# Kernel optimization log

Measured on AMD Instinct MI355X. Metric: run time of the kernel, lower is better.

Reference implementation:

```python
import jax, jax.numpy as jnp
import numpy as np

N_NODES = 50000
N_EDGES = 625000
D_IN = 128
D_OUT = 128


def setup_inputs() -> dict:
    key = jax.random.key(0)
    k1, k2, k3 = jax.random.split(key, 3)
    x = jax.random.normal(k1, (N_NODES, D_IN), dtype=jnp.float32)
    edge_index = jax.random.randint(k2, (2, N_EDGES), 0, N_NODES, dtype=jnp.int64)
    # torch Linear weight: [d_out, d_in], Kaiming-uniform-ish scale
    weight = jax.random.normal(k3, (D_OUT, D_IN), dtype=jnp.float32) * (1.0 / np.sqrt(D_IN))
    bias = jnp.zeros((D_OUT,), dtype=jnp.float32)
    return {"x": x, "edge_index": edge_index, "weight": weight, "bias": bias}


def reference(x, edge_index, weight, bias):
    N = x.shape[0]
    # gcn_norm: add self-loops with weight 1.0 (improved=False)
    loop = jnp.arange(N, dtype=edge_index.dtype)
    src = jnp.concatenate([edge_index[0], loop])  # [E+N] message sources (x_j)
    dst = jnp.concatenate([edge_index[1], loop])  # [E+N] aggregation targets
    ew = jnp.ones(src.shape[0], dtype=x.dtype)
    # degree computed on target index (col), symmetric normalization
    deg = jax.ops.segment_sum(ew, dst, num_segments=N)
    dinv = jnp.where(deg > 0, jax.lax.rsqrt(deg), 0.0).astype(x.dtype)
    norm = dinv[src] * ew * dinv[dst]  # [E+N]
    # message: norm_e * x[src]; aggregate: scatter-add at dst
    agg = jax.ops.segment_sum(norm[:, None] * x[src], dst, num_segments=N)  # [N, d_in]
    # Linear
    return agg @ weight.T + bias
```

## Files before the change

kernel.cpp:

```cpp
#include <hip/hip_runtime.h>
#include <hip/hip_bf16.h>

#define N_NODES 50000
#define N_EDGES 625000
#define D 128
#define CAP 64
#define NTILES ((N_NODES + 15) / 16)
#define NRANGE 8
#define RSPAN (N_NODES / NRANGE)
#define FILL_BLOCKS 1024
#define XW_BLOCKS 1024
#define PSTRIDE ((FILL_BLOCKS / NRANGE) * 256)

typedef __attribute__((ext_vector_type(8))) short bf16x8;
typedef __attribute__((ext_vector_type(4))) float f32x4;

__device__ __forceinline__ float b2f(short s) {
    unsigned u = ((unsigned)(unsigned short)s) << 16;
    return __uint_as_float(u);
}
__device__ __forceinline__ short f2b(float f) {
    union { __hip_bfloat16 h; short s; } cv;
    cv.h = __float2bfloat16(f);
    return cv.s;
}

__global__ void k_zero(int* __restrict__ deg) {
    int i = blockIdx.x * 256 + threadIdx.x;
    if (i < N_NODES) deg[i] = 0;
}

__global__ __launch_bounds__(256) void k_prep(const int* __restrict__ src,
                                              const int* __restrict__ dst,
                                              int* __restrict__ deg,
                                              unsigned short* __restrict__ colp,
                                              const float* __restrict__ x,
                                              const float* __restrict__ w,
                                              short* __restrict__ y) {
    int b = blockIdx.x;
    if (b < FILL_BLOCKS) {
        int g = b & 7;
        int bg = b >> 3;
        int lo = g * RSPAN, hi = lo + RSPAN;
        for (int e = bg * 256 + threadIdx.x; e < N_EDGES; e += PSTRIDE) {
            int d = dst[e];
            if (d >= lo && d < hi) {
                int p = atomicAdd(&deg[d], 1);
                if (p < CAP) colp[d * CAP + p] = (unsigned short)src[e];
            }
        }
    } else {
        int t = threadIdx.x;
        int wave = t >> 6, lane = t & 63;
        int c0 = wave * 32;
        int lr = lane & 15;
        int lk = (lane >> 4) * 8;

        bf16x8 wf0[4], wf1[4];
        {
            const float* wp0 = w + (size_t)(c0 + lr) * D + lk;
            const float* wp1 = wp0 + 16 * D;
            #pragma unroll
            for (int ks = 0; ks < 4; ++ks) {
                f32x4 wa0 = *(const f32x4*)(wp0 + ks * 32);
                f32x4 wb0 = *(const f32x4*)(wp0 + ks * 32 + 4);
                f32x4 wa1 = *(const f32x4*)(wp1 + ks * 32);
                f32x4 wb1 = *(const f32x4*)(wp1 + ks * 32 + 4);
                #pragma unroll
                for (int q = 0; q < 4; ++q) {
                    wf0[ks][q] = f2b(wa0[q]); wf0[ks][q + 4] = f2b(wb0[q]);
                    wf1[ks][q] = f2b(wa1[q]); wf1[ks][q + 4] = f2b(wb1[q]);
                }
            }
        }

        for (int tile = b - FILL_BLOCKS; tile < NTILES; tile += XW_BLOCKS) {
            int row0 = tile * 16;
            const float* ap = x + (size_t)(row0 + lr) * D + lk;
            f32x4 acc0 = {0.f, 0.f, 0.f, 0.f};
            f32x4 acc1 = {0.f, 0.f, 0.f, 0.f};
            #pragma unroll
            for (int ks = 0; ks < 4; ++ks) {
                f32x4 xa = *(const f32x4*)(ap + ks * 32);
                f32x4 xb = *(const f32x4*)(ap + ks * 32 + 4);
                bf16x8 a;
                #pragma unroll
                for (int q = 0; q < 4; ++q) { a[q] = f2b(xa[q]); a[q + 4] = f2b(xb[q]); }
                acc0 = __builtin_amdgcn_mfma_f32_16x16x32_bf16(a, wf0[ks], acc0, 0, 0, 0);
                acc1 = __builtin_amdgcn_mfma_f32_16x16x32_bf16(a, wf1[ks], acc1, 0, 0, 0);
            }
            int orow = row0 + (lane >> 4) * 4;
            int oc0 = c0 + lr, oc1 = c0 + 16 + lr;
            #pragma unroll
            for (int i = 0; i < 4; ++i) {
                y[(size_t)(orow + i) * D + oc0] = f2b(acc0[i]);
                y[(size_t)(orow + i) * D + oc1] = f2b(acc1[i]);
            }
        }
    }
}

__global__ __launch_bounds__(256) void k_gather(const short* __restrict__ y,
                                                const int* __restrict__ deg,
                                                const unsigned short* __restrict__ colp,
                                                const float* __restrict__ bias,
                                                float* __restrict__ out) {
    int tid = blockIdx.x * 256 + threadIdx.x;
    int n = tid >> 4;
    int sub = threadIdx.x & 15;
    int lane = threadIdx.x & 63;
    int gb = lane & 48;
    if (n >= N_NODES) return;
    int dn_raw = deg[n];
    float dd = rsqrtf((float)(dn_raw + 1));
    int dn = dn_raw < CAP ? dn_raw : CAP;
    bf16x8 self = *(const bf16x8*)(y + (size_t)n * D + sub * 8);
    float acc0[8], acc1[8];
    #pragma unroll
    for (int q = 0; q < 8; ++q) { acc0[q] = dd * b2f(self[q]); acc1[q] = 0.f; }
    const unsigned short* cp = colp + (size_t)n * CAP;

    for (int bj = 0; bj < dn; bj += 16) {
        int rem = dn - bj;
        int m = rem < 16 ? rem : 16;
        int cidx = 0;
        float cds = 0.f;
        if (sub < m) {
            cidx = cp[bj + sub];
            cds = rsqrtf((float)(deg[cidx] + 1));
        }
        int j = 0;
        for (; j + 4 <= m; j += 4) {
            int s0 = __shfl(cidx, gb + j + 0);
            int s1 = __shfl(cidx, gb + j + 1);
            int s2 = __shfl(cidx, gb + j + 2);
            int s3 = __shfl(cidx, gb + j + 3);
            float d0 = __shfl(cds, gb + j + 0);
            float d1 = __shfl(cds, gb + j + 1);
            float d2 = __shfl(cds, gb + j + 2);
            float d3 = __shfl(cds, gb + j + 3);
            bf16x8 v0 = *(const bf16x8*)(y + (size_t)s0 * D + sub * 8);
            bf16x8 v1 = *(const bf16x8*)(y + (size_t)s1 * D + sub * 8);
            bf16x8 v2 = *(const bf16x8*)(y + (size_t)s2 * D + sub * 8);
            bf16x8 v3 = *(const bf16x8*)(y + (size_t)s3 * D + sub * 8);
            #pragma unroll
            for (int q = 0; q < 8; ++q) {
                acc0[q] += d0 * b2f(v0[q]) + d2 * b2f(v2[q]);
                acc1[q] += d1 * b2f(v1[q]) + d3 * b2f(v3[q]);
            }
        }
        for (; j < m; ++j) {
            int s0 = __shfl(cidx, gb + j);
            float d0 = __shfl(cds, gb + j);
            bf16x8 v0 = *(const bf16x8*)(y + (size_t)s0 * D + sub * 8);
            #pragma unroll
            for (int q = 0; q < 8; ++q) acc0[q] += d0 * b2f(v0[q]);
        }
    }

    const float4* bch = (const float4*)(bias + sub * 8);
    float4 bb0 = bch[0], bb1 = bch[1];
    float4 o0, o1;
    o0.x = dd * (acc0[0] + acc1[0]) + bb0.x; o0.y = dd * (acc0[1] + acc1[1]) + bb0.y;
    o0.z = dd * (acc0[2] + acc1[2]) + bb0.z; o0.w = dd * (acc0[3] + acc1[3]) + bb0.w;
    o1.x = dd * (acc0[4] + acc1[4]) + bb1.x; o1.y = dd * (acc0[5] + acc1[5]) + bb1.y;
    o1.z = dd * (acc0[6] + acc1[6]) + bb1.z; o1.w = dd * (acc0[7] + acc1[7]) + bb1.w;
    float4* op = (float4*)(out + (size_t)n * D + sub * 8);
    op[0] = o0; op[1] = o1;
}

extern "C" void kernel_launch(void* const* d_in, const int* in_sizes, int n_in,
                              void* d_out, int out_size, void* d_ws, size_t ws_size,
                              hipStream_t stream) {
    const float* x    = (const float*)d_in[0];
    const int*   ei   = (const int*)d_in[1];
    const float* w    = (const float*)d_in[2];
    const float* bias = (const float*)d_in[3];
    float* out = (float*)d_out;

    const int* src = ei;
    const int* dst = ei + N_EDGES;

    char* p = (char*)d_ws;
    short* y  = (short*)p;             p += (size_t)N_NODES * D * 2;
    int* deg  = (int*)p;               p += (size_t)N_NODES * 4;
    unsigned short* colp = (unsigned short*)p;
    p += (size_t)N_NODES * CAP * 2;

    k_zero<<<(N_NODES + 255) / 256, 256, 0, stream>>>(deg);
    k_prep<<<FILL_BLOCKS + XW_BLOCKS, 256, 0, stream>>>(src, dst, deg, colp, x, w, y);
    k_gather<<<((N_NODES * 16) + 255) / 256, 256, 0, stream>>>(y, deg, colp, bias, out);
}
```

Measured before the change: 77.17 us.

## Assign edge-fill destination ranges by XCC with dynamic chunk work-stealing

The CSR fill phase used a static assignment where block b handled destination range b&7. Each fill block now reads its hardware XCC id and starts with the matching destination range, so the atomics on deg and the colp writes for a range stay mostly in one XCC's L2. Blocks take 2048-edge chunks from a per-range atomic cursor and move on to the other ranges when theirs is done, which balances load. The cost is extra global atomics and two barriers per chunk, and every block may end up scanning edges for several ranges.

```diff
diff --git a/kernel.cpp b/kernel.cpp
--- a/kernel.cpp
+++ b/kernel.cpp
@@ -10,7 +10,8 @@
 #define RSPAN (N_NODES / NRANGE)
 #define FILL_BLOCKS 1024
 #define XW_BLOCKS 1024
-#define PSTRIDE ((FILL_BLOCKS / NRANGE) * 256)
+#define CHUNK 2048
+#define NCHUNK ((N_EDGES + CHUNK - 1) / CHUNK)
 
 typedef __attribute__((ext_vector_type(8))) short bf16x8;
 typedef __attribute__((ext_vector_type(4))) float f32x4;
@@ -25,28 +26,47 @@
     return cv.s;
 }
 
-__global__ void k_zero(int* __restrict__ deg) {
+__global__ void k_zero(int* __restrict__ deg, int* __restrict__ cursor) {
     int i = blockIdx.x * 256 + threadIdx.x;
     if (i < N_NODES) deg[i] = 0;
+    if (i < NRANGE) cursor[i] = 0;
 }
 
 __global__ __launch_bounds__(256) void k_prep(const int* __restrict__ src,
                                               const int* __restrict__ dst,
                                               int* __restrict__ deg,
                                               unsigned short* __restrict__ colp,
+                                              int* __restrict__ cursor,
                                               const float* __restrict__ x,
                                               const float* __restrict__ w,
                                               short* __restrict__ y) {
     int b = blockIdx.x;
     if (b < FILL_BLOCKS) {
-        int g = b & 7;
-        int bg = b >> 3;
-        int lo = g * RSPAN, hi = lo + RSPAN;
-        for (int e = bg * 256 + threadIdx.x; e < N_EDGES; e += PSTRIDE) {
-            int d = dst[e];
-            if (d >= lo && d < hi) {
-                int p = atomicAdd(&deg[d], 1);
-                if (p < CAP) colp[d * CAP + p] = (unsigned short)src[e];
+        unsigned xcc;
+        asm volatile("s_getreg_b32 %0, hwreg(HW_REG_XCC_ID)" : "=s"(xcc));
+        int myg = (int)(xcc & 7u);
+        __shared__ int s_c;
+        for (int gi = 0; gi < NRANGE; ++gi) {
+            int g = (myg + gi) & 7;
+            int lo = g * RSPAN, hi = lo + RSPAN;
+            for (;;) {
+                if (threadIdx.x == 0) s_c = atomicAdd(&cursor[g], 1);
+                __syncthreads();
+                int c = s_c;
+                __syncthreads();
+                if (c >= NCHUNK) break;
+                int e0 = c * CHUNK + threadIdx.x;
+                #pragma unroll
+                for (int k = 0; k < CHUNK / 256; ++k) {
+                    int e = e0 + k * 256;
+                    if (e < N_EDGES) {
+                        int d = dst[e];
+                        if (d >= lo && d < hi) {
+                            int p = atomicAdd(&deg[d], 1);
+                            if (p < CAP) colp[d * CAP + p] = (unsigned short)src[e];
+                        }
+                    }
+                }
             }
         }
     } else {
@@ -186,8 +206,9 @@
     int* deg  = (int*)p;               p += (size_t)N_NODES * 4;
     unsigned short* colp = (unsigned short*)p;
     p += (size_t)N_NODES * CAP * 2;
-
-    k_zero<<<(N_NODES + 255) / 256, 256, 0, stream>>>(deg);
-    k_prep<<<FILL_BLOCKS + XW_BLOCKS, 256, 0, stream>>>(src, dst, deg, colp, x, w, y);
+    int* cursor = (int*)p;             p += 64 * 4;
+
+    k_zero<<<(N_NODES + 255) / 256, 256, 0, stream>>>(deg, cursor);
+    k_prep<<<FILL_BLOCKS + XW_BLOCKS, 256, 0, stream>>>(src, dst, deg, colp, cursor, x, w, y);
     k_gather<<<((N_NODES * 16) + 255) / 256, 256, 0, stream>>>(y, deg, colp, bias, out);
 }
```

Measured after the change: 182.4 us. 136% more time.
